# Kernel optimization log

Measured on AMD Instinct MI355X. Metric: run time of the kernel, lower is better.

## Reference

```python
import jax, jax.numpy as jnp
import numpy as np

KERNEL_SIZE = 11
OUT_CH = 512
IN_CH = 512


def make_pos_grid(k):
    # centered integer offsets, grid flattened at the end: shape (2, k*k)
    coords = jnp.arange(k, dtype=jnp.float32) - (k - 1) / 2.0
    yy, xx = jnp.meshgrid(coords, coords, indexing="ij")
    return jnp.stack([yy.reshape(-1), xx.reshape(-1)], axis=0)  # (2, k*k)


def setup_inputs() -> dict:
    key = jax.random.key(0)
    k1, _ = jax.random.split(key)
    # raw Cholesky parameters per (out_channel, in_channel) pair; diagonal goes
    # through exp() in reference() to guarantee positive-definite covariances.
    chol_raw = 0.1 * jax.random.normal(k1, (OUT_CH, IN_CH, 2, 2), dtype=jnp.float32)
    pos_grid = make_pos_grid(KERNEL_SIZE)
    return {"chol_raw": chol_raw, "pos_grid": pos_grid}


def reference(chol_raw, pos_grid):
    # chol_raw: (O, I, 2, 2) raw params; pos_grid: (2, K) with K = k*k
    O, I = chol_raw.shape[0], chol_raw.shape[1]
    K = pos_grid.shape[-1]
    k = int(round(np.sqrt(K)))

    # Lower-triangular Cholesky factor with positive diagonal:
    # L = [[exp(a), 0], [c, exp(d)]]
    l11 = jnp.exp(chol_raw[..., 0, 0])[..., None]  # (O, I, 1)
    l21 = chol_raw[..., 1, 0][..., None]           # (O, I, 1)
    l22 = jnp.exp(chol_raw[..., 1, 1])[..., None]  # (O, I, 1)

    x1 = pos_grid[0]  # (K,)
    x2 = pos_grid[1]  # (K,)

    # Inlined forward substitution: solve L b = x for each (o, i, position)
    b1 = x1 / l11                    # (O, I, K)
    b2 = (x2 - l21 * b1) / l22       # (O, I, K)

    # dists = sum over the 2-vector of squares = x^T S^{-1} x
    dists = (b1 * b1 + b2 * b2).reshape((O, I, k, k))
    return dists
```

## Files before the change

### kernel.cpp

```cpp
#include <hip/hip_runtime.h>

#define KK 121
#define NPAIR (512 * 512)
#define PPB 64
#define NBLK (NPAIR / PPB)
#define STAGE_F4 (PPB * KK / 4)

__global__ __launch_bounds__(256) void
quad_rank3_kernel(const float4* __restrict__ chol4,
                  const float* __restrict__ pg,
                  float4* __restrict__ out4) {
    __shared__ float4 s_uvw[KK];
    __shared__ __align__(16) float stage[PPB * KK];

    const int t = threadIdx.x;

    if (t < KK) {
        float x1 = pg[t];
        float x2 = pg[KK + t];
        float4 g;
        g.x = x1 * x1; g.y = x2 * x2; g.z = x1 * x2; g.w = 0.f;
        s_uvw[t] = g;
    }

    const int p       = t & 63;
    const int quarter = t >> 6;
    const int k0 = (quarter == 0) ? 0 : (30 * quarter + 1);
    const int k1 = (quarter == 0) ? 31 : (k0 + 30);

    float4 c = chol4[blockIdx.x * PPB + p];
    float e1 = __expf(-c.x);
    float e2 = __expf(-c.w);
    float f  = c.z * e2;
    float P  = e1 * e1 * fmaf(f, f, 1.f);
    float Q  = e2 * e2;
    float R  = -2.f * f * e1 * e2;

    __syncthreads();

    float* st = &stage[p * KK];
#pragma unroll 5
    for (int k = k0; k < k1; ++k) {
        float4 g = s_uvw[k];
        st[k] = fmaf(P, g.x, fmaf(Q, g.y, R * g.z));
    }

    __syncthreads();

    const float4* s4 = (const float4*)stage;
    float4* o = out4 + (size_t)blockIdx.x * STAGE_F4;
#pragma unroll
    for (int i = t; i < STAGE_F4; i += 256) {
        o[i] = s4[i];
    }
}

extern "C" void kernel_launch(void* const* d_in, const int* in_sizes, int n_in,
                              void* d_out, int out_size, void* d_ws, size_t ws_size,
                              hipStream_t stream) {
    const float4* chol4 = (const float4*)d_in[0];
    const float* pg     = (const float*)d_in[1];
    float4* out4        = (float4*)d_out;

    quad_rank3_kernel<<<NBLK, 256, 0, stream>>>(chol4, pg, out4);
}
```

Baseline: 131.6 us.

## Make kernel persistent with double-buffered LDS staging and nontemporal stores

Replaces the one-block-per-64-pairs launch with a fixed grid of 512 persistent blocks, each looping over 8 chunks. The LDS staging buffer is double-buffered, so the next chunk's compute can overlap the previous chunk's copy-out with a single barrier per iteration. Output stores become nontemporal to avoid cache pollution on the write-only stream. LDS use doubles per block, which may reduce occupancy.

```diff
diff --git a/kernel.cpp b/kernel.cpp
--- a/kernel.cpp
+++ b/kernel.cpp
@@ -3,22 +3,26 @@
 #define KK 121
 #define NPAIR (512 * 512)
 #define PPB 64
-#define NBLK (NPAIR / PPB)
+#define NCHUNK (NPAIR / PPB)
+#define GRID 512
+#define CPB (NCHUNK / GRID)
 #define STAGE_F4 (PPB * KK / 4)
 
+typedef float vf4 __attribute__((ext_vector_type(4)));
+
 __global__ __launch_bounds__(256) void
-quad_rank3_kernel(const float4* __restrict__ chol4,
-                  const float* __restrict__ pg,
-                  float4* __restrict__ out4) {
-    __shared__ float4 s_uvw[KK];
-    __shared__ __align__(16) float stage[PPB * KK];
+quad_persist_kernel(const vf4* __restrict__ chol4,
+                    const float* __restrict__ pg,
+                    vf4* __restrict__ out4) {
+    __shared__ vf4 s_uvw[KK];
+    __shared__ __align__(16) float stage[2][PPB * KK];
 
     const int t = threadIdx.x;
 
     if (t < KK) {
         float x1 = pg[t];
         float x2 = pg[KK + t];
-        float4 g;
+        vf4 g;
         g.x = x1 * x1; g.y = x2 * x2; g.z = x1 * x2; g.w = 0.f;
         s_uvw[t] = g;
     }
@@ -28,39 +32,43 @@
     const int k0 = (quarter == 0) ? 0 : (30 * quarter + 1);
     const int k1 = (quarter == 0) ? 31 : (k0 + 30);
 
-    float4 c = chol4[blockIdx.x * PPB + p];
-    float e1 = __expf(-c.x);
-    float e2 = __expf(-c.w);
-    float f  = c.z * e2;
-    float P  = e1 * e1 * fmaf(f, f, 1.f);
-    float Q  = e2 * e2;
-    float R  = -2.f * f * e1 * e2;
-
     __syncthreads();
 
-    float* st = &stage[p * KK];
+    for (int c = 0; c < CPB; ++c) {
+        const int chunk = blockIdx.x * CPB + c;
+
+        vf4 cc = chol4[chunk * PPB + p];
+        float e1 = __expf(-cc.x);
+        float e2 = __expf(-cc.w);
+        float f  = cc.z * e2;
+        float P  = e1 * e1 * fmaf(f, f, 1.f);
+        float Q  = e2 * e2;
+        float R  = -2.f * f * e1 * e2;
+
+        float* st = &stage[c & 1][p * KK];
 #pragma unroll 5
-    for (int k = k0; k < k1; ++k) {
-        float4 g = s_uvw[k];
-        st[k] = fmaf(P, g.x, fmaf(Q, g.y, R * g.z));
-    }
+        for (int k = k0; k < k1; ++k) {
+            vf4 g = s_uvw[k];
+            st[k] = fmaf(P, g.x, fmaf(Q, g.y, R * g.z));
+        }
 
-    __syncthreads();
+        __syncthreads();
 
-    const float4* s4 = (const float4*)stage;
-    float4* o = out4 + (size_t)blockIdx.x * STAGE_F4;
+        const vf4* s4 = (const vf4*)stage[c & 1];
+        vf4* o = out4 + (size_t)chunk * STAGE_F4;
 #pragma unroll
-    for (int i = t; i < STAGE_F4; i += 256) {
-        o[i] = s4[i];
+        for (int i = t; i < STAGE_F4; i += 256) {
+            __builtin_nontemporal_store(s4[i], &o[i]);
+        }
     }
 }
 
 extern "C" void kernel_launch(void* const* d_in, const int* in_sizes, int n_in,
                               void* d_out, int out_size, void* d_ws, size_t ws_size,
                               hipStream_t stream) {
-    const float4* chol4 = (const float4*)d_in[0];
-    const float* pg     = (const float*)d_in[1];
-    float4* out4        = (float4*)d_out;
+    const vf4* chol4 = (const vf4*)d_in[0];
+    const float* pg  = (const float*)d_in[1];
+    vf4* out4        = (vf4*)d_out;
 
-    quad_rank3_kernel<<<NBLK, 256, 0, stream>>>(chol4, pg, out4);
+    quad_persist_kernel<<<GRID, 256, 0, stream>>>(chol4, pg, out4);
 }
```

New measurement: 141.0 us. +7.1%, slower.
